# Kernel optimization log

Hardware: AMD Instinct MI355X
Metric: run time of the kernel (lower is better)

## Reference

```python
import jax, jax.numpy as jnp
import numpy as np


def _conv(x, w, pad, groups=1):
    # NCHW conv, OIHW weights, stride 1
    return jax.lax.conv_general_dilated(
        x, w, (1, 1), [(pad, pad), (pad, pad)],
        dimension_numbers=('NCHW', 'OIHW', 'NCHW'),
        feature_group_count=groups)


def setup_inputs() -> dict:
    key = jax.random.key(0)
    ks = jax.random.split(key, 16)
    b, c, h, w = 4, 64, 256, 256
    heads = 8
    s = 0.05
    inp = {
        'x': jax.random.normal(ks[0], (b, c, h, w), jnp.float32),
        # qkv 1x1 conv (with bias) then depthwise 3x3 (with bias)
        'w_qkv': jax.random.normal(ks[1], (3 * c, c, 1, 1), jnp.float32) * s,
        'b_qkv': jax.random.normal(ks[2], (3 * c,), jnp.float32) * s,
        'w_dw': jax.random.normal(ks[3], (3 * c, 1, 3, 3), jnp.float32) * s,
        'b_dw': jax.random.normal(ks[4], (3 * c,), jnp.float32) * s,
        # project_out 1x1 (with bias)
        'w_proj': jax.random.normal(ks[5], (c, c, 1, 1), jnp.float32) * s,
        'b_proj': jax.random.normal(ks[6], (c,), jnp.float32) * s,
        'temperature': jnp.ones((heads, 1, 1), jnp.float32),
        # V_MaskAttention.conv2: 1x1(no bias) -> BN -> 5x5 pad2(no bias)
        'w_m1': jax.random.normal(ks[7], (c, c, 1, 1), jnp.float32) * s,
        'bn_gamma': jnp.ones((c,), jnp.float32),
        'bn_beta': jnp.zeros((c,), jnp.float32),
        'bn_mean': jax.random.normal(ks[8], (c,), jnp.float32) * 0.1,
        'bn_var': jax.random.uniform(ks[9], (c,), jnp.float32, 0.5, 1.5),
        'w_m2': jax.random.normal(ks[10], (c, c, 5, 5), jnp.float32) * s,
    }
    return inp


def reference(x, w_qkv, b_qkv, w_dw, b_dw, w_proj, b_proj, temperature,
              w_m1, bn_gamma, bn_beta, bn_mean, bn_var, w_m2):
    b, c, h, w = x.shape
    heads = temperature.shape[0]

    # qkv conv1x1 + depthwise 3x3 (v chunk computed but unused, as in source)
    qkv = _conv(x, w_qkv, 0) + b_qkv[None, :, None, None]
    qkv = _conv(qkv, w_dw, 1, groups=3 * c) + b_dw[None, :, None, None]
    q, k, _ = jnp.split(qkv, 3, axis=1)

    # V_MaskAttention gated value path (BN in eval mode, eps=1e-5)
    y = _conv(x, w_m1, 0)
    y = (y - bn_mean[None, :, None, None]) * (
        bn_gamma[None, :, None, None]
        / jnp.sqrt(bn_var[None, :, None, None] + 1e-5)) + bn_beta[None, :, None, None]
    x2 = jax.nn.sigmoid(_conv(y, w_m2, 2))
    v = x + x * x2

    def heads_view(t):  # b,(head c),h,w -> b,head,c_head,hw
        return t.reshape(b, heads, c // heads, h * w)

    q = heads_view(q)
    k = heads_view(k)
    v = heads_view(v)

    # L2 normalize over spatial dim (torch F.normalize eps=1e-12)
    q = q / jnp.maximum(jnp.linalg.norm(q, axis=-1, keepdims=True), 1e-12)
    k = k / jnp.maximum(jnp.linalg.norm(k, axis=-1, keepdims=True), 1e-12)

    attn = jnp.einsum('bhcn,bhdn->bhcd', q, k) * temperature[None]  # [b,h,c',c']
    attn = jax.nn.softmax(attn, axis=-1)
    out = jnp.einsum('bhcd,bhdn->bhcn', attn, v).reshape(b, c, h, w)
    return _conv(out, w_proj, 0) + b_proj[None, :, None, None]
```

## Files before the change

kernel.cpp:

```cpp
#include <hip/hip_runtime.h>
#include <math.h>

#define B 4
#define C 64
#define NN 65536

typedef __attribute__((ext_vector_type(8))) short short8;
typedef __attribute__((ext_vector_type(4))) short short4b;
typedef __attribute__((ext_vector_type(4))) float f32x4;
typedef __attribute__((ext_vector_type(4))) unsigned int u32x4;

__device__ inline float bf2f(short s) {
  union { unsigned u; float f; } v; v.u = ((unsigned)(unsigned short)s) << 16; return v.f;
}
__device__ inline short f2bf(float f) {
  union { float f; unsigned u; } v; v.f = f;
  unsigned r = v.u + 0x7FFFu + ((v.u >> 16) & 1u);
  return (short)(r >> 16);
}
__device__ inline float lof(unsigned u) {
  union { unsigned u; float f; } v; v.u = u << 16; return v.f;
}
__device__ inline float hif(unsigned u) {
  union { unsigned u; float f; } v; v.u = u & 0xffff0000u; return v.f;
}

__global__ __launch_bounds__(256) void k_xt(const float* __restrict__ x,
    short* __restrict__ x_t, const float* __restrict__ wqkv,
    const float* __restrict__ wm1, short* __restrict__ apk,
    short* __restrict__ apm, float* __restrict__ gram2) {
  if (blockIdx.x >= 1024) {
    const int bid = blockIdx.x - 1024;
    for (int idx = bid * 256 + threadIdx.x; idx < 20480; idx += 16384) {
      if (idx < 8192) {
        const int j = idx & 7, lane = (idx >> 3) & 63, mt = (idx >> 9) & 7, cc = idx >> 12;
        const int o = mt * 16 + (lane & 15), c = cc * 32 + (lane >> 4) * 8 + j;
        apk[idx] = f2bf(wqkv[o * 64 + c]);
      } else if (idx < 12288) {
        const int k = idx - 8192;
        const int j = k & 7, lane = (k >> 3) & 63, mt = (k >> 9) & 3, cc = k >> 11;
        const int o = mt * 16 + (lane & 15), c = cc * 32 + (lane >> 4) * 8 + j;
        apm[k] = f2bf(wm1[o * 64 + c]);
      } else {
        gram2[idx - 12288] = 0.f;
      }
    }
    return;
  }
  __shared__ short lds[256 * 66];
  const int b = blockIdx.x >> 8, n0 = (blockIdx.x & 255) << 8;
  const int t = threadIdx.x;
#pragma unroll 4
  for (int c = 0; c < 64; ++c)
    lds[t * 66 + c] = f2bf(x[((size_t)(b * 64 + c)) * NN + n0 + t]);
  __syncthreads();
  short* dst = x_t + ((size_t)(b * NN + n0)) * 64;
#pragma unroll
  for (int it = 0; it < 8; ++it) {
    const int idx = it * 256 + t;
    const int nl = idx >> 3, cb = idx & 7;
    *(short8*)(dst + (size_t)nl * 64 + cb * 8) = *(const short8*)(lds + nl * 66 + cb * 8);
  }
}

__global__ __launch_bounds__(256, 4) void k_qk1x1(const short* __restrict__ x_t,
    const short* __restrict__ apk, const float* __restrict__ bias,
    short* __restrict__ qk) {
  const int b = blockIdx.x >> 10, ntile = blockIdx.x & 1023;
  const int wave = threadIdx.x >> 6, lane = threadIdx.x & 63;
  const int quad = lane >> 4, l15 = lane & 15;
  const int n = ntile * 64 + wave * 16 + l15;
  f32x4 acc[8];
#pragma unroll
  for (int mt = 0; mt < 8; ++mt) acc[mt] = (f32x4){0.f, 0.f, 0.f, 0.f};
#pragma unroll
  for (int cc = 0; cc < 2; ++cc) {
    const short8 bf = *(const short8*)(x_t + ((size_t)(b * NN + n)) * 64 + cc * 32 + quad * 8);
#pragma unroll
    for (int mt = 0; mt < 8; ++mt) {
      const short8 af = *(const short8*)(apk + ((cc * 8 + mt) * 64 + lane) * 8);
      acc[mt] = __builtin_amdgcn_mfma_f32_16x16x32_bf16(af, bf, acc[mt], 0, 0, 0);
    }
  }
#pragma unroll
  for (int mt = 0; mt < 8; ++mt)
#pragma unroll
    for (int reg = 0; reg < 4; ++reg) {
      const int o = mt * 16 + quad * 4 + reg;
      qk[((size_t)(b * 128 + o)) * NN + n] = f2bf(acc[mt][reg] + bias[o]);
    }
}

__global__ __launch_bounds__(256, 3) void k_gram(const short* __restrict__ qk,
    const float* __restrict__ wdw, const float* __restrict__ bdw,
    float* __restrict__ gram2) {
  __shared__ float red[4][256];
  const int bh = blockIdx.x >> 6, chunk = blockIdx.x & 63;
  const int b = bh >> 3, h = bh & 7;
  const int wave = threadIdx.x >> 6, lane = threadIdx.x & 63;
  const int quad = lane >> 4, l15 = lane & 15;
  const int ch = (l15 < 8) ? (h * 8 + l15) : (64 + h * 8 + (l15 - 8));
  const short* plane = qk + ((size_t)(b * 128 + ch)) * NN;
  float wreg[9];
#pragma unroll
  for (int i = 0; i < 9; ++i) wreg[i] = wdw[ch * 9 + i];
  const float bias = bdw[ch];
  const int row = chunk * 4 + wave;
  const short* prow = plane + row * 256;
  u32x4 rb[3][8];
#pragma unroll
  for (int dy = 0; dy < 3; ++dy) {
    if (dy == 0 && row == 0) continue;
    if (dy == 2 && row == 255) continue;
    const short* pr = prow + (dy - 1) * 256 + quad * 8;
#pragma unroll
    for (int s = 0; s < 8; ++s)
      rb[dy][s] = *(const u32x4*)(pr + s * 32);
  }
  f32x4 acc = {0.f, 0.f, 0.f, 0.f};
#pragma unroll
  for (int s = 0; s < 8; ++s) {
    float a[8];
#pragma unroll
    for (int j = 0; j < 8; ++j) a[j] = bias;
#pragma unroll
    for (int dy = 0; dy < 3; ++dy) {
      if (dy == 0 && row == 0) continue;
      if (dy == 2 && row == 255) continue;
      const unsigned w0_ = rb[dy][s][0], w1_ = rb[dy][s][1],
                     w2_ = rb[dy][s][2], w3_ = rb[dy][s][3];
      float m[10];
      m[1] = lof(w0_); m[2] = hif(w0_);
      m[3] = lof(w1_); m[4] = hif(w1_);
      m[5] = lof(w2_); m[6] = hif(w2_);
      m[7] = lof(w3_); m[8] = hif(w3_);
      unsigned m0w, m9w;
      if (s == 0) {
        m0w = (unsigned)__shfl((int)w3_, (lane - 16) & 63, 64);
      } else {
        const unsigned w3sel = (quad == 3) ? rb[dy][s - 1][3] : w3_;
        m0w = (unsigned)__shfl((int)w3sel, (lane - 16) & 63, 64);
      }
      if (s == 7) {
        m9w = (unsigned)__shfl((int)w0_, (lane + 16) & 63, 64);
      } else {
        const unsigned w0sel = (quad == 0) ? rb[dy][s + 1][0] : w0_;
        m9w = (unsigned)__shfl((int)w0sel, (lane + 16) & 63, 64);
      }
      m[0] = (s == 0 && quad == 0) ? 0.f : hif(m0w);
      m[9] = (s == 7 && quad == 3) ? 0.f : lof(m9w);
      const float W0 = wreg[dy * 3], W1 = wreg[dy * 3 + 1], W2 = wreg[dy * 3 + 2];
#pragma unroll
      for (int j = 0; j < 8; ++j)
        a[j] = fmaf(W2, m[j + 2], fmaf(W1, m[j + 1], fmaf(W0, m[j], a[j])));
    }
    short8 frag;
#pragma unroll
    for (int j = 0; j < 8; ++j) frag[j] = f2bf(a[j]);
    acc = __builtin_amdgcn_mfma_f32_16x16x32_bf16(frag, frag, acc, 0, 0, 0);
  }
#pragma unroll
  for (int reg = 0; reg < 4; ++reg)
    red[wave][(quad * 4 + reg) * 16 + l15] = acc[reg];
  __syncthreads();
  {
    const int e = threadIdx.x;
    const float s4 = red[0][e] + red[1][e] + red[2][e] + red[3][e];
    atomicAdd(&gram2[bh * 256 + e], s4);
  }
}

__global__ __launch_bounds__(256, 4) void k_m1_bn(const short* __restrict__ x_t,
    const short* __restrict__ apm, const float* __restrict__ gamma,
    const float* __restrict__ beta, const float* __restrict__ mean,
    const float* __restrict__ var, short* __restrict__ y_t,
    const float* __restrict__ w2, short* __restrict__ apw2) {
  if (blockIdx.x >= 4096) {
    const int bid = blockIdx.x - 4096;
    for (int idx = bid * 256 + threadIdx.x; idx < 25 * 2 * 4 * 64 * 8; idx += 16384) {
      const int j = idx & 7, lane = (idx >> 3) & 63, mt = (idx >> 9) & 3,
                cc = (idx >> 11) & 1, t = idx >> 12;
      const int o = mt * 16 + (lane & 15);
      const int c = cc * 32 + (lane >> 4) * 8 + j;
      apw2[idx] = f2bf(w2[((size_t)o * 64 + c) * 25 + t]);
    }
    return;
  }
  __shared__ short lds[64 * 66];
  const int b = blockIdx.x >> 10, ntile = blockIdx.x & 1023;
  const int wave = threadIdx.x >> 6, lane = threadIdx.x & 63;
  const int quad = lane >> 4, l15 = lane & 15;
  const int n = ntile * 64 + wave * 16 + l15;
  f32x4 acc[4];
#pragma unroll
  for (int mt = 0; mt < 4; ++mt) acc[mt] = (f32x4){0.f, 0.f, 0.f, 0.f};
#pragma unroll
  for (int cc = 0; cc < 2; ++cc) {
    const short8 bf = *(const short8*)(x_t + ((size_t)(b * NN + n)) * 64 + cc * 32 + quad * 8);
#pragma unroll
    for (int mt = 0; mt < 4; ++mt) {
      const short8 af = *(const short8*)(apm + ((cc * 4 + mt) * 64 + lane) * 8);
      acc[mt] = __builtin_amdgcn_mfma_f32_16x16x32_bf16(af, bf, acc[mt], 0, 0, 0);
    }
  }
#pragma unroll
  for (int mt = 0; mt < 4; ++mt)
#pragma unroll
    for (int reg = 0; reg < 4; ++reg) {
      const int o = mt * 16 + quad * 4 + reg;
      const float sc = gamma[o] * rsqrtf(var[o] + 1e-5f);
      lds[(wave * 16 + l15) * 66 + o] = f2bf((acc[mt][reg] - mean[o]) * sc + beta[o]);
    }
  __syncthreads();
  short* dst = y_t + ((size_t)(b * NN + ntile * 64)) * 64;
#pragma unroll
  for (int it = 0; it < 2; ++it) {
    const int idx = it * 256 + threadIdx.x;
    const int lcol = idx >> 3, cb = idx & 7;
    *(short8*)(dst + (size_t)lcol * 64 + cb * 8) = *(const short8*)(lds + lcol * 66 + cb * 8);
  }
}

__global__ __launch_bounds__(256, 2) void k_conv5(const short* __restrict__ y_t,
    const short* __restrict__ apw2, const short* __restrict__ x_t,
    short* __restrict__ v_t) {
  __shared__ short slds[8 * 64 * 76];
  char* sb = (char*)slds;
  const int b = blockIdx.x >> 7;
  const int rg = (blockIdx.x >> 2) & 31, cg = blockIdx.x & 3;
  const int r0 = rg * 8, x0 = cg * 64;
  const int wave = threadIdx.x >> 6, lane = threadIdx.x & 63;
  const int quad = lane >> 4, l15 = lane & 15;
  f32x4 acc[4][2][4];
#pragma unroll
  for (int mt = 0; mt < 4; ++mt)
#pragma unroll
    for (int r = 0; r < 2; ++r)
#pragma unroll
      for (int nt = 0; nt < 4; ++nt) acc[mt][r][nt] = (f32x4){0.f, 0.f, 0.f, 0.f};
  for (int cc = 0; cc < 2; ++cc) {
    if (cc) __syncthreads();
    for (int idx = threadIdx.x; idx < 12 * 68 * 4; idx += 256) {
      const int rr = idx / 272, rem = idx - rr * 272;
      const int col = rem >> 2, cb = rem & 3;
      const int gr = r0 - 2 + rr, gc = x0 - 2 + col;
      short8 val = {0, 0, 0, 0, 0, 0, 0, 0};
      if (gr >= 0 && gr < 256 && gc >= 0 && gc < 256)
        val = *(const short8*)(y_t + ((size_t)(b * NN + gr * 256 + gc)) * 64 + cc * 32 + cb * 8);
      const int L = rr * 68 + col;
      *(short8*)(sb + ((L * 64 + cb * 16) ^ (((L >> 1) & 3) << 4))) = val;
    }
    __syncthreads();
    for (int t = 0; t < 25; ++t) {
      const int dy = t / 5 - 2, dx = t % 5 - 2;
      short8 a[4];
#pragma unroll
      for (int mt = 0; mt < 4; ++mt)
        a[mt] = *(const short8*)(apw2 + (((t * 2 + cc) * 4 + mt) * 64 + lane) * 8);
#pragma unroll
      for (int r = 0; r < 2; ++r) {
        const int rr = wave * 2 + r + 2 + dy;
#pragma unroll
        for (int nt = 0; nt < 4; ++nt) {
          const int L = rr * 68 + nt * 16 + l15 + 2 + dx;
          const short8 bf =
              *(const short8*)(sb + ((L * 64 + quad * 16) ^ (((L >> 1) & 3) << 4)));
#pragma unroll
          for (int mt = 0; mt < 4; ++mt)
            acc[mt][r][nt] =
                __builtin_amdgcn_mfma_f32_16x16x32_bf16(a[mt], bf, acc[mt][r][nt], 0, 0, 0);
        }
      }
    }
  }
  __syncthreads();
#pragma unroll
  for (int r = 0; r < 2; ++r) {
    const int lrow = wave * 2 + r;
    const int row = r0 + lrow;
#pragma unroll
    for (int nt = 0; nt < 4; ++nt) {
      const int lcol = nt * 16 + l15;
      const short* xp = x_t + ((size_t)(b * NN + row * 256 + x0 + lcol)) * 64 + quad * 4;
#pragma unroll
      for (int mt = 0; mt < 4; ++mt) {
        const short4b xv4 = *(const short4b*)(xp + mt * 16);
        short4b pk;
#pragma unroll
        for (int reg = 0; reg < 4; ++reg) {
          const float sg = 1.f / (1.f + __expf(-acc[mt][r][nt][reg]));
          pk[reg] = f2bf(bf2f(xv4[reg]) * (1.f + sg));
        }
        *(short4b*)(slds + (lrow * 64 + lcol) * 76 + mt * 16 + quad * 4) = pk;
      }
    }
  }
  __syncthreads();
#pragma unroll
  for (int it = 0; it < 16; ++it) {
    const int idx = it * 256 + threadIdx.x;
    const int cb = idx & 7, lcol = (idx >> 3) & 63, rr = idx >> 9;
    *(short8*)(v_t + ((size_t)(b * NN + (r0 + rr) * 256 + x0 + lcol)) * 64 + cb * 8) =
        *(const short8*)(slds + (rr * 64 + lcol) * 76 + cb * 8);
  }
}

__global__ __launch_bounds__(256) void k_attn_e(const float* __restrict__ gram2,
    const float* __restrict__ temp, const float* __restrict__ wproj,
    short* __restrict__ Epack) {
  __shared__ float attn[2048];
  const int t = threadIdx.x;
  {
    const int b = t >> 6, h = (t >> 3) & 7, c = t & 7;
    const float* g = gram2 + (b * 8 + h) * 256;
    const float qn = fmaxf(sqrtf(g[c * 16 + c]), 1e-12f);
    const float tp = temp[h];
    float row[8];
    float mx = -1e30f;
#pragma unroll
    for (int d = 0; d < 8; ++d) {
      const float kn = fmaxf(sqrtf(g[(8 + d) * 16 + (8 + d)]), 1e-12f);
      row[d] = g[c * 16 + 8 + d] / (qn * kn) * tp;
      mx = fmaxf(mx, row[d]);
    }
    float s = 0.f;
#pragma unroll
    for (int d = 0; d < 8; ++d) { row[d] = __expf(row[d] - mx); s += row[d]; }
    const float inv = 1.f / s;
#pragma unroll
    for (int d = 0; d < 8; ++d) attn[t * 8 + d] = row[d] * inv;
  }
  __syncthreads();
  for (int idx = blockIdx.x * 1024 + t; idx < (blockIdx.x + 1) * 1024; idx += 256) {
    const int j = idx & 7, lane = (idx >> 3) & 63, mt = (idx >> 9) & 3,
              cc = (idx >> 11) & 1, b = idx >> 12;
    const int o = mt * 16 + (lane & 15);
    const int cv = cc * 32 + (lane >> 4) * 8 + j;
    const int h = cv >> 3, d = cv & 7;
    float a = 0.f;
#pragma unroll
    for (int c2 = 0; c2 < 8; ++c2)
      a += wproj[o * 64 + h * 8 + c2] * attn[((b * 8 + h) * 8 + c2) * 8 + d];
    Epack[idx] = f2bf(a);
  }
}

__global__ __launch_bounds__(256, 4) void k_out(const short* __restrict__ v_t,
    const short* __restrict__ Epack, const float* __restrict__ bproj,
    float* __restrict__ out) {
  const int b = blockIdx.x >> 10, ntile = blockIdx.x & 1023;
  const int wave = threadIdx.x >> 6, lane = threadIdx.x & 63;
  const int quad = lane >> 4, l15 = lane & 15;
  const int n = ntile * 64 + wave * 16 + l15;
  f32x4 acc[4];
#pragma unroll
  for (int mt = 0; mt < 4; ++mt) acc[mt] = (f32x4){0.f, 0.f, 0.f, 0.f};
#pragma unroll
  for (int cc = 0; cc < 2; ++cc) {
    const short8 bf = *(const short8*)(v_t + ((size_t)(b * NN + n)) * 64 + cc * 32 + quad * 8);
#pragma unroll
    for (int mt = 0; mt < 4; ++mt) {
      const short8 af = *(const short8*)(Epack + (((b * 2 + cc) * 4 + mt) * 64 + lane) * 8);
      acc[mt] = __builtin_amdgcn_mfma_f32_16x16x32_bf16(af, bf, acc[mt], 0, 0, 0);
    }
  }
#pragma unroll
  for (int mt = 0; mt < 4; ++mt)
#pragma unroll
    for (int reg = 0; reg < 4; ++reg) {
      const int o = mt * 16 + quad * 4 + reg;
      out[((size_t)(b * 64 + o)) * NN + n] = acc[mt][reg] + bproj[o];
    }
}

extern "C" void kernel_launch(void* const* d_in, const int* in_sizes, int n_in,
                              void* d_out, int out_size, void* d_ws, size_t ws_size,
                              hipStream_t stream) {
  const float* x     = (const float*)d_in[0];
  const float* wqkv  = (const float*)d_in[1];
  const float* bqkv  = (const float*)d_in[2];
  const float* wdw   = (const float*)d_in[3];
  const float* bdw   = (const float*)d_in[4];
  const float* wproj = (const float*)d_in[5];
  const float* bproj = (const float*)d_in[6];
  const float* temp  = (const float*)d_in[7];
  const float* wm1   = (const float*)d_in[8];
  const float* gamma = (const float*)d_in[9];
  const float* beta  = (const float*)d_in[10];
  const float* mean  = (const float*)d_in[11];
  const float* var   = (const float*)d_in[12];
  const float* wm2   = (const float*)d_in[13];

  char* wsb = (char*)d_ws;
  short* qk    = (short*)(wsb);
  short* v_t   = (short*)(wsb);
  short* apw2  = (short*)(wsb + 33554432);
  short* x_t   = (short*)(wsb + 67108864);
  short* y_t   = (short*)(wsb + 100663296);
  float* gram2 = (float*)(wsb + 134217728);
  short* apk   = (short*)(wsb + 134217728 + 32768);
  short* apm   = (short*)(wsb + 134217728 + 49152);
  short* Epack = (short*)(wsb + 134217728 + 57344);
  float* out   = (float*)d_out;

  k_xt<<<dim3(1088), dim3(256), 0, stream>>>(x, x_t, wqkv, wm1, apk, apm, gram2);
  k_qk1x1<<<dim3(4096), dim3(256), 0, stream>>>(x_t, apk, bqkv, qk);
  k_gram<<<dim3(2048), dim3(256), 0, stream>>>(qk, wdw, bdw, gram2);
  k_m1_bn<<<dim3(4160), dim3(256), 0, stream>>>(x_t, apm, gamma, beta, mean, var, y_t,
                                                wm2, apw2);
  k_conv5<<<dim3(512), dim3(256), 0, stream>>>(y_t, apw2, x_t, v_t);
  k_attn_e<<<dim3(16), dim3(256), 0, stream>>>(gram2, temp, wproj, Epack);
  k_out<<<dim3(4096), dim3(256), 0, stream>>>(v_t, Epack, bproj, out);
}
```

Measured before the change: 293.5 us.

## Fuse transpose, qk 1x1 conv, and m1+BN into one kernel; merge prep kernels

Merges the x transpose/bf16 cast, the qkv 1x1 MFMA conv and the m1 1x1 conv with BN into one kernel per 64-pixel tile. Both GEMMs read x from LDS instead of re-reading x_t from global memory twice. Weight packing is split into a small prep kernel, and the conv5 weight pack is merged with the attention/Epack computation into one launch, which removes a launch. The cost is more register and LDS pressure in the fused kernel, which could lower occupancy.

New measurement: 288.3 us. About the same (-1.8%).

```diff
diff --git a/kernel.cpp b/kernel.cpp
--- a/kernel.cpp
+++ b/kernel.cpp
@@ -25,70 +25,106 @@
   union { unsigned u; float f; } v; v.u = u & 0xffff0000u; return v.f;
 }
 
-__global__ __launch_bounds__(256) void k_xt(const float* __restrict__ x,
-    short* __restrict__ x_t, const float* __restrict__ wqkv,
-    const float* __restrict__ wm1, short* __restrict__ apk,
-    short* __restrict__ apm, float* __restrict__ gram2) {
-  if (blockIdx.x >= 1024) {
-    const int bid = blockIdx.x - 1024;
-    for (int idx = bid * 256 + threadIdx.x; idx < 20480; idx += 16384) {
-      if (idx < 8192) {
-        const int j = idx & 7, lane = (idx >> 3) & 63, mt = (idx >> 9) & 7, cc = idx >> 12;
-        const int o = mt * 16 + (lane & 15), c = cc * 32 + (lane >> 4) * 8 + j;
-        apk[idx] = f2bf(wqkv[o * 64 + c]);
-      } else if (idx < 12288) {
-        const int k = idx - 8192;
-        const int j = k & 7, lane = (k >> 3) & 63, mt = (k >> 9) & 3, cc = k >> 11;
-        const int o = mt * 16 + (lane & 15), c = cc * 32 + (lane >> 4) * 8 + j;
-        apm[k] = f2bf(wm1[o * 64 + c]);
-      } else {
-        gram2[idx - 12288] = 0.f;
-      }
-    }
-    return;
-  }
-  __shared__ short lds[256 * 66];
-  const int b = blockIdx.x >> 8, n0 = (blockIdx.x & 255) << 8;
+__global__ void k_prep1(const float* __restrict__ wqkv, const float* __restrict__ wm1,
+    short* __restrict__ apk, short* __restrict__ apm, float* __restrict__ gram2) {
+  for (int idx = blockIdx.x * 256 + threadIdx.x; idx < 20480; idx += 16384) {
+    if (idx < 8192) {
+      const int j = idx & 7, lane = (idx >> 3) & 63, mt = (idx >> 9) & 7, cc = idx >> 12;
+      const int o = mt * 16 + (lane & 15), c = cc * 32 + (lane >> 4) * 8 + j;
+      apk[idx] = f2bf(wqkv[o * 64 + c]);
+    } else if (idx < 12288) {
+      const int k = idx - 8192;
+      const int j = k & 7, lane = (k >> 3) & 63, mt = (k >> 9) & 3, cc = k >> 11;
+      const int o = mt * 16 + (lane & 15), c = cc * 32 + (lane >> 4) * 8 + j;
+      apm[k] = f2bf(wm1[o * 64 + c]);
+    } else {
+      gram2[idx - 12288] = 0.f;
+    }
+  }
+}
+
+__global__ __launch_bounds__(256, 4) void k_fused(const float* __restrict__ x,
+    const short* __restrict__ apk, const float* __restrict__ bqkv,
+    const short* __restrict__ apm, const float* __restrict__ gamma,
+    const float* __restrict__ beta, const float* __restrict__ mean,
+    const float* __restrict__ var, short* __restrict__ x_t,
+    short* __restrict__ qk, short* __restrict__ y_t) {
+  __shared__ short lds[64 * 66];
+  const int b = blockIdx.x >> 10, ntile = blockIdx.x & 1023;
+  const int n0 = ntile * 64;
   const int t = threadIdx.x;
-#pragma unroll 4
-  for (int c = 0; c < 64; ++c)
-    lds[t * 66 + c] = f2bf(x[((size_t)(b * 64 + c)) * NN + n0 + t]);
-  __syncthreads();
-  short* dst = x_t + ((size_t)(b * NN + n0)) * 64;
-#pragma unroll
-  for (int it = 0; it < 8; ++it) {
+  const int wave = t >> 6, lane = t & 63;
+  const int quad = lane >> 4, l15 = lane & 15;
+#pragma unroll
+  for (int it = 0; it < 16; ++it) {
     const int idx = it * 256 + t;
-    const int nl = idx >> 3, cb = idx & 7;
-    *(short8*)(dst + (size_t)nl * 64 + cb * 8) = *(const short8*)(lds + nl * 66 + cb * 8);
-  }
-}
-
-__global__ __launch_bounds__(256, 4) void k_qk1x1(const short* __restrict__ x_t,
-    const short* __restrict__ apk, const float* __restrict__ bias,
-    short* __restrict__ qk) {
-  const int b = blockIdx.x >> 10, ntile = blockIdx.x & 1023;
-  const int wave = threadIdx.x >> 6, lane = threadIdx.x & 63;
-  const int quad = lane >> 4, l15 = lane & 15;
-  const int n = ntile * 64 + wave * 16 + l15;
-  f32x4 acc[8];
-#pragma unroll
-  for (int mt = 0; mt < 8; ++mt) acc[mt] = (f32x4){0.f, 0.f, 0.f, 0.f};
+    const int c = idx >> 6, nl = idx & 63;
+    lds[nl * 66 + c] = f2bf(x[((size_t)(b * 64 + c)) * NN + n0 + nl]);
+  }
+  __syncthreads();
+  {
+    short* dst = x_t + ((size_t)(b * NN + n0)) * 64;
+#pragma unroll
+    for (int it = 0; it < 2; ++it) {
+      const int idx = it * 256 + t;
+      const int nl = idx >> 3, cb = idx & 7;
+      *(short8*)(dst + (size_t)nl * 64 + cb * 8) = *(const short8*)(lds + nl * 66 + cb * 8);
+    }
+  }
+  const int nloc = wave * 16 + l15;
+  const int n = n0 + nloc;
+  {
+    f32x4 acc[8];
+#pragma unroll
+    for (int mt = 0; mt < 8; ++mt) acc[mt] = (f32x4){0.f, 0.f, 0.f, 0.f};
+#pragma unroll
+    for (int cc = 0; cc < 2; ++cc) {
+      const short8 bf = *(const short8*)(lds + nloc * 66 + cc * 32 + quad * 8);
+#pragma unroll
+      for (int mt = 0; mt < 8; ++mt) {
+        const short8 af = *(const short8*)(apk + ((cc * 8 + mt) * 64 + lane) * 8);
+        acc[mt] = __builtin_amdgcn_mfma_f32_16x16x32_bf16(af, bf, acc[mt], 0, 0, 0);
+      }
+    }
+#pragma unroll
+    for (int mt = 0; mt < 8; ++mt)
+#pragma unroll
+      for (int reg = 0; reg < 4; ++reg) {
+        const int o = mt * 16 + quad * 4 + reg;
+        qk[((size_t)(b * 128 + o)) * NN + n] = f2bf(acc[mt][reg] + bqkv[o]);
+      }
+  }
+  f32x4 acc2[4];
+#pragma unroll
+  for (int mt = 0; mt < 4; ++mt) acc2[mt] = (f32x4){0.f, 0.f, 0.f, 0.f};
 #pragma unroll
   for (int cc = 0; cc < 2; ++cc) {
-    const short8 bf = *(const short8*)(x_t + ((size_t)(b * NN + n)) * 64 + cc * 32 + quad * 8);
-#pragma unroll
-    for (int mt = 0; mt < 8; ++mt) {
-      const short8 af = *(const short8*)(apk + ((cc * 8 + mt) * 64 + lane) * 8);
-      acc[mt] = __builtin_amdgcn_mfma_f32_16x16x32_bf16(af, bf, acc[mt], 0, 0, 0);
-    }
-  }
-#pragma unroll
-  for (int mt = 0; mt < 8; ++mt)
+    const short8 bf = *(const short8*)(lds + nloc * 66 + cc * 32 + quad * 8);
+#pragma unroll
+    for (int mt = 0; mt < 4; ++mt) {
+      const short8 af = *(const short8*)(apm + ((cc * 4 + mt) * 64 + lane) * 8);
+      acc2[mt] = __builtin_amdgcn_mfma_f32_16x16x32_bf16(af, bf, acc2[mt], 0, 0, 0);
+    }
+  }
+  __syncthreads();
+#pragma unroll
+  for (int mt = 0; mt < 4; ++mt)
 #pragma unroll
     for (int reg = 0; reg < 4; ++reg) {
       const int o = mt * 16 + quad * 4 + reg;
-      qk[((size_t)(b * 128 + o)) * NN + n] = f2bf(acc[mt][reg] + bias[o]);
-    }
+      const float sc = gamma[o] * rsqrtf(var[o] + 1e-5f);
+      lds[nloc * 66 + o] = f2bf((acc2[mt][reg] - mean[o]) * sc + beta[o]);
+    }
+  __syncthreads();
+  {
+    short* dst = y_t + ((size_t)(b * NN + n0)) * 64;
+#pragma unroll
+    for (int it = 0; it < 2; ++it) {
+      const int idx = it * 256 + t;
+      const int nl = idx >> 3, cb = idx & 7;
+      *(short8*)(dst + (size_t)nl * 64 + cb * 8) = *(const short8*)(lds + nl * 66 + cb * 8);
+    }
+  }
 }
 
 __global__ __launch_bounds__(256, 3) void k_gram(const short* __restrict__ qk,
@@ -170,14 +206,12 @@
   }
 }
 
-__global__ __launch_bounds__(256, 4) void k_m1_bn(const short* __restrict__ x_t,
-    const short* __restrict__ apm, const float* __restrict__ gamma,
-    const float* __restrict__ beta, const float* __restrict__ mean,
-    const float* __restrict__ var, short* __restrict__ y_t,
-    const float* __restrict__ w2, short* __restrict__ apw2) {
-  if (blockIdx.x >= 4096) {
-    const int bid = blockIdx.x - 4096;
-    for (int idx = bid * 256 + threadIdx.x; idx < 25 * 2 * 4 * 64 * 8; idx += 16384) {
+__global__ __launch_bounds__(256) void k_prep2e(const float* __restrict__ w2,
+    short* __restrict__ apw2, const float* __restrict__ gram2,
+    const float* __restrict__ temp, const float* __restrict__ wproj,
+    short* __restrict__ Epack) {
+  if (blockIdx.x < 64) {
+    for (int idx = blockIdx.x * 256 + threadIdx.x; idx < 25 * 2 * 4 * 64 * 8; idx += 16384) {
       const int j = idx & 7, lane = (idx >> 3) & 63, mt = (idx >> 9) & 3,
                 cc = (idx >> 11) & 1, t = idx >> 12;
       const int o = mt * 16 + (lane & 15);
@@ -186,38 +220,41 @@
     }
     return;
   }
-  __shared__ short lds[64 * 66];
-  const int b = blockIdx.x >> 10, ntile = blockIdx.x & 1023;
-  const int wave = threadIdx.x >> 6, lane = threadIdx.x & 63;
-  const int quad = lane >> 4, l15 = lane & 15;
-  const int n = ntile * 64 + wave * 16 + l15;
-  f32x4 acc[4];
-#pragma unroll
-  for (int mt = 0; mt < 4; ++mt) acc[mt] = (f32x4){0.f, 0.f, 0.f, 0.f};
-#pragma unroll
-  for (int cc = 0; cc < 2; ++cc) {
-    const short8 bf = *(const short8*)(x_t + ((size_t)(b * NN + n)) * 64 + cc * 32 + quad * 8);
-#pragma unroll
-    for (int mt = 0; mt < 4; ++mt) {
-      const short8 af = *(const short8*)(apm + ((cc * 4 + mt) * 64 + lane) * 8);
-      acc[mt] = __builtin_amdgcn_mfma_f32_16x16x32_bf16(af, bf, acc[mt], 0, 0, 0);
-    }
-  }
-#pragma unroll
-  for (int mt = 0; mt < 4; ++mt)
-#pragma unroll
-    for (int reg = 0; reg < 4; ++reg) {
-      const int o = mt * 16 + quad * 4 + reg;
-      const float sc = gamma[o] * rsqrtf(var[o] + 1e-5f);
-      lds[(wave * 16 + l15) * 66 + o] = f2bf((acc[mt][reg] - mean[o]) * sc + beta[o]);
-    }
-  __syncthreads();
-  short* dst = y_t + ((size_t)(b * NN + ntile * 64)) * 64;
-#pragma unroll
-  for (int it = 0; it < 2; ++it) {
-    const int idx = it * 256 + threadIdx.x;
-    const int lcol = idx >> 3, cb = idx & 7;
-    *(short8*)(dst + (size_t)lcol * 64 + cb * 8) = *(const short8*)(lds + lcol * 66 + cb * 8);
+  const int bid = blockIdx.x - 64;
+  __shared__ float attn[2048];
+  const int t = threadIdx.x;
+  {
+    const int b = t >> 6, h = (t >> 3) & 7, c = t & 7;
+    const float* g = gram2 + (b * 8 + h) * 256;
+    const float qn = fmaxf(sqrtf(g[c * 16 + c]), 1e-12f);
+    const float tp = temp[h];
+    float row[8];
+    float mx = -1e30f;
+#pragma unroll
+    for (int d = 0; d < 8; ++d) {
+      const float kn = fmaxf(sqrtf(g[(8 + d) * 16 + (8 + d)]), 1e-12f);
+      row[d] = g[c * 16 + 8 + d] / (qn * kn) * tp;
+      mx = fmaxf(mx, row[d]);
+    }
+    float s = 0.f;
+#pragma unroll
+    for (int d = 0; d < 8; ++d) { row[d] = __expf(row[d] - mx); s += row[d]; }
+    const float inv = 1.f / s;
+#pragma unroll
+    for (int d = 0; d < 8; ++d) attn[t * 8 + d] = row[d] * inv;
+  }
+  __syncthreads();
+  for (int idx = bid * 1024 + t; idx < (bid + 1) * 1024; idx += 256) {
+    const int j = idx & 7, lane = (idx >> 3) & 63, mt = (idx >> 9) & 3,
+              cc = (idx >> 11) & 1, b = idx >> 12;
+    const int o = mt * 16 + (lane & 15);
+    const int cv = cc * 32 + (lane >> 4) * 8 + j;
+    const int h = cv >> 3, d = cv & 7;
+    float a = 0.f;
+#pragma unroll
+    for (int c2 = 0; c2 < 8; ++c2)
+      a += wproj[o * 64 + h * 8 + c2] * attn[((b * 8 + h) * 8 + c2) * 8 + d];
+    Epack[idx] = f2bf(a);
   }
 }
 
@@ -302,46 +339,6 @@
     const int cb = idx & 7, lcol = (idx >> 3) & 63, rr = idx >> 9;
     *(short8*)(v_t + ((size_t)(b * NN + (r0 + rr) * 256 + x0 + lcol)) * 64 + cb * 8) =
         *(const short8*)(slds + (rr * 64 + lcol) * 76 + cb * 8);
-  }
-}
-
-__global__ __launch_bounds__(256) void k_attn_e(const float* __restrict__ gram2,
-    const float* __restrict__ temp, const float* __restrict__ wproj,
-    short* __restrict__ Epack) {
-  __shared__ float attn[2048];
-  const int t = threadIdx.x;
-  {
-    const int b = t >> 6, h = (t >> 3) & 7, c = t & 7;
-    const float* g = gram2 + (b * 8 + h) * 256;
-    const float qn = fmaxf(sqrtf(g[c * 16 + c]), 1e-12f);
-    const float tp = temp[h];
-    float row[8];
-    float mx = -1e30f;
-#pragma unroll
-    for (int d = 0; d < 8; ++d) {
-      const float kn = fmaxf(sqrtf(g[(8 + d) * 16 + (8 + d)]), 1e-12f);
-      row[d] = g[c * 16 + 8 + d] / (qn * kn) * tp;
-      mx = fmaxf(mx, row[d]);
-    }
-    float s = 0.f;
-#pragma unroll
-    for (int d = 0; d < 8; ++d) { row[d] = __expf(row[d] - mx); s += row[d]; }
-    const float inv = 1.f / s;
-#pragma unroll
-    for (int d = 0; d < 8; ++d) attn[t * 8 + d] = row[d] * inv;
-  }
-  __syncthreads();
-  for (int idx = blockIdx.x * 1024 + t; idx < (blockIdx.x + 1) * 1024; idx += 256) {
-    const int j = idx & 7, lane = (idx >> 3) & 63, mt = (idx >> 9) & 3,
-              cc = (idx >> 11) & 1, b = idx >> 12;
-    const int o = mt * 16 + (lane & 15);
-    const int cv = cc * 32 + (lane >> 4) * 8 + j;
-    const int h = cv >> 3, d = cv & 7;
-    float a = 0.f;
-#pragma unroll
-    for (int c2 = 0; c2 < 8; ++c2)
-      a += wproj[o * 64 + h * 8 + c2] * attn[((b * 8 + h) * 8 + c2) * 8 + d];
-    Epack[idx] = f2bf(a);
   }
 }
 
@@ -403,12 +400,11 @@
   short* Epack = (short*)(wsb + 134217728 + 57344);
   float* out   = (float*)d_out;
 
-  k_xt<<<dim3(1088), dim3(256), 0, stream>>>(x, x_t, wqkv, wm1, apk, apm, gram2);
-  k_qk1x1<<<dim3(4096), dim3(256), 0, stream>>>(x_t, apk, bqkv, qk);
+  k_prep1<<<dim3(64), dim3(256), 0, stream>>>(wqkv, wm1, apk, apm, gram2);
+  k_fused<<<dim3(4096), dim3(256), 0, stream>>>(x, apk, bqkv, apm, gamma, beta,
+                                                mean, var, x_t, qk, y_t);
   k_gram<<<dim3(2048), dim3(256), 0, stream>>>(qk, wdw, bdw, gram2);
-  k_m1_bn<<<dim3(4160), dim3(256), 0, stream>>>(x_t, apm, gamma, beta, mean, var, y_t,
-                                                wm2, apw2);
+  k_prep2e<<<dim3(80), dim3(256), 0, stream>>>(wm2, apw2, gram2, temp, wproj, Epack);
   k_conv5<<<dim3(512), dim3(256), 0, stream>>>(y_t, apw2, x_t, v_t);
-  k_attn_e<<<dim3(16), dim3(256), 0, stream>>>(gram2, temp, wproj, Epack);
   k_out<<<dim3(4096), dim3(256), 0, stream>>>(v_t, Epack, bproj, out);
 }
```
